# Performance work log

Measured on AMD Instinct MI355X. Metric: run time of the kernel, lower is better.

Reference implementation:

```python
import jax, jax.numpy as jnp
import numpy as np

N_STATE, N_CTRL, T, NB = 32, 16, 128, 64
NSC = N_STATE + N_CTRL

mT = lambda m: jnp.swapaxes(m, -1, -2)


def setup_inputs() -> dict:
    key = jax.random.key(0)
    k1, k2, k3, k4, k5, k6 = jax.random.split(key, 6)
    # Q must be PSD (the torch example builds Q = Qr^T Qr); add I for conditioning.
    Qr = jax.random.normal(k1, (NB, T, NSC, NSC), jnp.float32)
    Q = mT(Qr) @ Qr / NSC + jnp.eye(NSC, dtype=jnp.float32)
    p = jax.random.normal(k2, (NB, T, NSC), jnp.float32)
    x_init = jax.random.normal(k3, (NB, N_STATE), jnp.float32)
    # Stable-ish linear dynamics so the T=128 rollout does not blow up.
    A = jnp.tile(0.95 * jnp.eye(N_STATE, dtype=jnp.float32), (NB, 1, 1)) \
        + 0.02 * jax.random.normal(k4, (NB, N_STATE, N_STATE), jnp.float32)
    Bm = 0.1 * jax.random.normal(k5, (NB, N_STATE, N_CTRL), jnp.float32)
    c1 = 0.1 * jax.random.normal(k6, (NB, N_STATE), jnp.float32)
    return {"x_init": x_init, "Q": Q, "p": p, "A": A, "Bm": Bm, "c1": c1}


def _gains(Qt, qt, ns):
    # Qt: [B, nsc, nsc], qt: [B, nsc, 1]
    Qxx, Qxu = Qt[:, :ns, :ns], Qt[:, :ns, ns:]
    Qux, Quu = Qt[:, ns:, :ns], Qt[:, ns:, ns:]
    qx, qu = qt[:, :ns], qt[:, ns:]
    Quu_inv = jnp.linalg.pinv(Quu)          # batched pinv, as in the torch code
    K = -(Quu_inv @ Qux)                    # [B, nc, ns]
    k = -(Quu_inv @ qu)                     # [B, nc, 1]
    KT = mT(K)
    V = Qxx + Qxu @ K + KT @ Qux + KT @ Quu @ K
    v = qx + Qxu @ k + KT @ qu + KT @ Quu @ k
    return K, k, V, v


def _lqr(x_init, Q, p, A, Bm, c1):
    ns = A.shape[-1]
    F = jnp.concatenate([A, Bm], axis=-1)   # [B, ns, nsc]
    FT = mT(F)
    ft = c1[..., None]                       # [B, ns, 1]

    # ---- backward Riccati/DP recursion (sequential over T) ----
    K_last, k_last, V, v = _gains(Q[:, -1], p[:, -1][..., None], ns)

    def bstep(carry, inp):
        Vtp1, vtp1 = carry
        Qt_raw, pt = inp                     # [B,nsc,nsc], [B,nsc]
        Qt = Qt_raw + FT @ Vtp1 @ F
        qt = pt[..., None] + FT @ (Vtp1 @ ft) + FT @ vtp1
        K, k, Vt, vt = _gains(Qt, qt, ns)
        return (Vt, vt), (K, k)

    Qtm = jnp.swapaxes(Q[:, :-1], 0, 1)[::-1]   # [T-1, B, nsc, nsc], t = T-2..0
    ptm = jnp.swapaxes(p[:, :-1], 0, 1)[::-1]
    _, (Ks_rev, ks_rev) = jax.lax.scan(bstep, (V, v), (Qtm, ptm))
    Ks = jnp.concatenate([Ks_rev[::-1], K_last[None]], axis=0)  # [T, B, nc, ns], forward time order
    ks = jnp.concatenate([ks_rev[::-1], k_last[None]], axis=0)  # [T, B, nc, 1]

    # ---- forward rollout ----
    def fstep(x, inp):
        K, k, Qt, pt = inp
        u = jnp.einsum('bij,bj->bi', K, x) + k[..., 0]
        xu = jnp.concatenate([x, u], axis=-1)                 # tau_t, [B, nsc]
        obj = 0.5 * jnp.einsum('bi,bij,bj->b', xu, Qt, xu) + jnp.einsum('bi,bi->b', xu, pt)
        xn = jnp.einsum('bij,bj->bi', A, x) + jnp.einsum('bij,bj->bi', Bm, u) + c1
        return xn, (x, u, obj, xu)

    Qf = jnp.swapaxes(Q, 0, 1)               # [T, B, nsc, nsc]
    pf = jnp.swapaxes(p, 0, 1)
    _, (xs, us, objs, taus) = jax.lax.scan(fstep, x_init, (Ks, ks, Qf, pf))
    # xs: [T, B, ns] (x_0..x_{T-1}, matching torch which does not append x_T)
    return xs, us, objs, taus


def reference(x_init, Q, p, A, Bm, c1):
    return _lqr(x_init, Q, p, A, Bm, c1)
```

## Files before the change

kernel.cpp:

```cpp
#include <hip/hip_runtime.h>

#define TT     128
#define NBATCH 64

#define BAR()  asm volatile("s_waitcnt lgkmcnt(0)\n\ts_barrier" ::: "memory")
#define BARV() asm volatile("s_waitcnt vmcnt(0) lgkmcnt(0)\n\ts_barrier" ::: "memory")

__device__ __forceinline__ void gload16(const float* g, float* l) {
    __builtin_amdgcn_global_load_lds(
        (__attribute__((address_space(1))) void*)g,
        (__attribute__((address_space(3))) void*)l, 16, 0, 0);
}

__device__ __forceinline__ float rdlane(float v, int l) {
    return __int_as_float(__builtin_amdgcn_readlane(__float_as_int(v), l));
}

__device__ __forceinline__ void inv4(const float4 pr[4], float IP[4][4]) {
    float a00=pr[0].x, a01=pr[0].y, a10=pr[1].x, a11=pr[1].y;
    float b00=pr[0].z, b01=pr[0].w, b10=pr[1].z, b11=pr[1].w;
    float c00=pr[2].x, c01=pr[2].y, c10=pr[3].x, c11=pr[3].y;
    float d00=pr[2].z, d01=pr[2].w, d10=pr[3].z, d11=pr[3].w;
    float r = 1.0f / (a00*a11 - a01*a10);
    float ia00 =  a11*r, ia01 = -a01*r, ia10 = -a10*r, ia11 = a00*r;
    float t00 = ia00*b00 + ia01*b10, t01 = ia00*b01 + ia01*b11;
    float t10 = ia10*b00 + ia11*b10, t11 = ia10*b01 + ia11*b11;
    float u00 = c00*ia00 + c01*ia10, u01 = c00*ia01 + c01*ia11;
    float u10 = c10*ia00 + c11*ia10, u11 = c10*ia01 + c11*ia11;
    float s00 = d00 - (c00*t00 + c01*t10), s01 = d01 - (c00*t01 + c01*t11);
    float s10 = d10 - (c10*t00 + c11*t10), s11 = d11 - (c10*t01 + c11*t11);
    float rs = 1.0f / (s00*s11 - s01*s10);
    float is00 =  s11*rs, is01 = -s01*rs, is10 = -s10*rs, is11 = s00*rs;
    float su00 = is00*u00 + is01*u10, su01 = is00*u01 + is01*u11;
    float su10 = is10*u00 + is11*u10, su11 = is10*u01 + is11*u11;
    IP[0][0] = ia00 + (t00*su00 + t01*su10);
    IP[0][1] = ia01 + (t00*su01 + t01*su11);
    IP[1][0] = ia10 + (t10*su00 + t11*su10);
    IP[1][1] = ia11 + (t10*su01 + t11*su11);
    IP[0][2] = -(t00*is00 + t01*is10);  IP[0][3] = -(t00*is01 + t01*is11);
    IP[1][2] = -(t10*is00 + t11*is10);  IP[1][3] = -(t10*is01 + t11*is11);
    IP[2][0] = -su00; IP[2][1] = -su01;
    IP[3][0] = -su10; IP[3][1] = -su11;
    IP[2][2] = is00;  IP[2][3] = is01;
    IP[3][2] = is10;  IP[3][3] = is11;
}

__global__ __launch_bounds__(256, 1)
void lqr_backward(const float* __restrict__ Q, const float* __restrict__ p,
                  const float* __restrict__ A, const float* __restrict__ Bm,
                  const float* __restrict__ c1, float* __restrict__ Kws)
{
    const int b   = blockIdx.x;
    const int tid = threadIdx.x;

    __shared__ __align__(16) float Fs[32*52];
    __shared__ __align__(16) float Vs[32*36];
    __shared__ __align__(16) float Ms[32*52];
    __shared__ __align__(16) float Xs[48*52];
    __shared__ __align__(16) float Qtb[2][48*48];
    __shared__ __align__(16) float qtb[2][256];
    __shared__ __align__(16) float KKs[16*36];
    __shared__ float vsv[32], fts[32], wv[32];

    const int ar0 = (tid / 12) * 2, ac0 = (tid % 12) * 4;
    const int br0 = (tid / 12) * 4, bc0 = (tid % 12) * 4;
    const int pi  = (tid - 64) >> 2;
    const int pg  = (tid - 64) & 3;
    const int pj0 = pg * 8;

    for (int st = tid; st < 256; st += 256) {
        int k = st >> 3, q = st & 7;
        ((float4*)(Fs + k*52))[q] = ((const float4*)A)[(b*32 + k)*8 + q];
    }
    for (int st = tid; st < 128; st += 256) {
        int k = st >> 2, q = st & 3;
        ((float4*)(Fs + k*52))[8 + q] = ((const float4*)Bm)[(b*32 + k)*4 + q];
    }
    for (int st = tid; st < 288; st += 256) ((float4*)Vs)[st] = make_float4(0,0,0,0);
    if (tid < 32) { vsv[tid] = 0.0f; fts[tid] = c1[b*32 + tid]; }

    {
        const float* Qs0 = Q + (size_t)(b*TT + TT-1) * 2304;
        #pragma unroll
        for (int r = 0; r < 3; ++r) {
            int e = r*256 + tid;
            if (e < 576) gload16(Qs0 + e*4, Qtb[0] + e*4);
        }
        if (tid < 12) gload16(p + (size_t)(b*TT + TT-1)*48 + tid*4, qtb[0] + tid*4);
    }
    BARV();

    for (int t = TT-1; t >= 0; --t) {
        const int cur = (TT-1 - t) & 1;
        float* Qtc = Qtb[cur];
        float* qtc = qtb[cur];
        float* Kbase = Kws + (size_t)(b*TT + t) * 528;

        if (tid < 192) {
            float4 a0 = make_float4(0,0,0,0), a1 = a0;
            #pragma unroll
            for (int k = 0; k < 32; ++k) {
                float2 v = *(const float2*)(Vs + k*36 + ar0);
                float4 f = *(const float4*)(Fs + k*52 + ac0);
                a0.x += v.x*f.x; a0.y += v.x*f.y; a0.z += v.x*f.z; a0.w += v.x*f.w;
                a1.x += v.y*f.x; a1.y += v.y*f.y; a1.z += v.y*f.z; a1.w += v.y*f.w;
            }
            *(float4*)(Ms + (ar0  )*52 + ac0) = a0;
            *(float4*)(Ms + (ar0+1)*52 + ac0) = a1;
        } else {
            const int idx = tid - 192;
            if (t > 0) {
                const float* Qs = Q + (size_t)(b*TT + t-1) * 2304;
                float* dst = Qtb[cur ^ 1];
                #pragma unroll
                for (int r = 0; r < 9; ++r) {
                    int e = r*64 + idx;
                    gload16(Qs + e*4, dst + e*4);
                }
                if (idx < 12) gload16(p + (size_t)(b*TT + t-1)*48 + idx*4,
                                      qtb[cur ^ 1] + idx*4);
            }
            if (idx < 32) {
                float acc = vsv[idx];
                #pragma unroll
                for (int k = 0; k < 32; ++k) acc += Vs[idx*36 + k] * fts[k];
                wv[idx] = acc;
            }
        }
        BAR();

        if (tid < 144) {
            float4 a0 = *(const float4*)(Qtc + (br0+0)*48 + bc0);
            float4 a1 = *(const float4*)(Qtc + (br0+1)*48 + bc0);
            float4 a2 = *(const float4*)(Qtc + (br0+2)*48 + bc0);
            float4 a3 = *(const float4*)(Qtc + (br0+3)*48 + bc0);
            #pragma unroll
            for (int k = 0; k < 32; ++k) {
                float4 fr = *(const float4*)(Fs + k*52 + br0);
                float4 mc = *(const float4*)(Ms + k*52 + bc0);
                a0.x += fr.x*mc.x; a0.y += fr.x*mc.y; a0.z += fr.x*mc.z; a0.w += fr.x*mc.w;
                a1.x += fr.y*mc.x; a1.y += fr.y*mc.y; a1.z += fr.y*mc.z; a1.w += fr.y*mc.w;
                a2.x += fr.z*mc.x; a2.y += fr.z*mc.y; a2.z += fr.z*mc.z; a2.w += fr.z*mc.w;
                a3.x += fr.w*mc.x; a3.y += fr.w*mc.y; a3.z += fr.w*mc.z; a3.w += fr.w*mc.w;
            }
            *(float4*)(Xs + (br0+0)*52 + bc0) = a0;
            *(float4*)(Xs + (br0+1)*52 + bc0) = a1;
            *(float4*)(Xs + (br0+2)*52 + bc0) = a2;
            *(float4*)(Xs + (br0+3)*52 + bc0) = a3;
        } else if (tid >= 192 && tid < 240) {
            const int c = tid - 192;
            float acc = qtc[c];
            #pragma unroll
            for (int k = 0; k < 32; ++k) acc += Fs[k*52 + c] * wv[k];
            qtc[c] = acc;
            if (c >= 32) Xs[c*52 + 48] = acc;
        }
        BAR();

        float4 pa0, pa1; float pq[16];
        if (tid < 64) {
            const int c = (tid < 49) ? tid : 48;
            float col[16];
            #pragma unroll
            for (int r = 0; r < 16; ++r) col[r] = Xs[(32+r)*52 + c];

            #pragma unroll
            for (int q = 0; q < 4; ++q) {
                const int pc = 32 + 4*q;
                float4 pr[4];
                #pragma unroll
                for (int m = 0; m < 4; ++m) {
                    pr[m].x = rdlane(col[4*q+m], pc+0);
                    pr[m].y = rdlane(col[4*q+m], pc+1);
                    pr[m].z = rdlane(col[4*q+m], pc+2);
                    pr[m].w = rdlane(col[4*q+m], pc+3);
                }
                float IP[4][4];
                inv4(pr, IP);
                float R[4];
                #pragma unroll
                for (int m = 0; m < 4; ++m)
                    R[m] = IP[m][0]*col[4*q+0] + IP[m][1]*col[4*q+1]
                         + IP[m][2]*col[4*q+2] + IP[m][3]*col[4*q+3];
                #pragma unroll
                for (int r = 0; r < 16; ++r) {
                    if ((r >> 2) == q) continue;
                    float f0 = rdlane(col[r], pc+0);
                    float f1 = rdlane(col[r], pc+1);
                    float f2 = rdlane(col[r], pc+2);
                    float f3 = rdlane(col[r], pc+3);
                    col[r] -= f0*R[0] + f1*R[1] + f2*R[2] + f3*R[3];
                }
                #pragma unroll
                for (int m = 0; m < 4; ++m) col[4*q+m] = R[m];
            }

            if (tid < 32) {
                #pragma unroll
                for (int r = 0; r < 16; ++r) {
                    KKs[r*36 + c]    = col[r];
                    Kbase[c*16 + r]  = -col[r];
                }
            } else if (tid == 48) {
                #pragma unroll
                for (int r = 0; r < 16; ++r) {
                    KKs[r*36 + 32]   = col[r];
                    Kbase[512 + r]   = -col[r];
                }
            }
        } else if (tid < 192) {
            pa0 = *(const float4*)(Xs + pi*52 + pj0);
            pa1 = *(const float4*)(Xs + pi*52 + pj0 + 4);
            #pragma unroll
            for (int m = 0; m < 4; ++m) {
                float4 v4 = *(const float4*)(Xs + pi*52 + 32 + m*4);
                pq[m*4+0] = v4.x; pq[m*4+1] = v4.y;
                pq[m*4+2] = v4.z; pq[m*4+3] = v4.w;
            }
        }
        BAR();

        if (tid >= 64 && tid < 192) {
            #pragma unroll
            for (int k = 0; k < 16; ++k) {
                float4 k0 = *(const float4*)(KKs + k*36 + pj0);
                float4 k1 = *(const float4*)(KKs + k*36 + pj0 + 4);
                pa0.x -= pq[k]*k0.x; pa0.y -= pq[k]*k0.y;
                pa0.z -= pq[k]*k0.z; pa0.w -= pq[k]*k0.w;
                pa1.x -= pq[k]*k1.x; pa1.y -= pq[k]*k1.y;
                pa1.z -= pq[k]*k1.z; pa1.w -= pq[k]*k1.w;
            }
            *(float4*)(Vs + pi*36 + pj0)     = pa0;
            *(float4*)(Vs + pi*36 + pj0 + 4) = pa1;
            if (pg == 0) {
                float accv = qtc[pi];
                #pragma unroll
                for (int k = 0; k < 16; ++k) accv -= pq[k] * KKs[k*36 + 32];
                vsv[pi] = accv;
            }
        }
        BARV();
    }
}

__global__ __launch_bounds__(64, 1)
void lqr_forward(const float* __restrict__ Kws, const float* __restrict__ A,
                 const float* __restrict__ Bm, const float* __restrict__ c1,
                 const float* __restrict__ x_init,
                 float* __restrict__ xs, float* __restrict__ us,
                 float* __restrict__ taus)
{
    const int b = blockIdx.x, l = threadIdx.x;
    __shared__ __align__(16) float Fb[32*48];
    __shared__ __align__(16) float Kb[544];
    __shared__ float c1s[32], xu[48];

    for (int st = l; st < 256; st += 64) {
        int k = st >> 3, q = st & 7;
        ((float4*)Fb)[k*12 + q] = ((const float4*)A)[(b*32 + k)*8 + q];
    }
    for (int st = l; st < 128; st += 64) {
        int k = st >> 2, q = st & 3;
        ((float4*)Fb)[k*12 + 8 + q] = ((const float4*)Bm)[(b*32 + k)*4 + q];
    }
    if (l < 32) { c1s[l] = c1[b*32 + l]; xu[l] = x_init[b*32 + l]; }

    float4 ka, kb, kc = make_float4(0,0,0,0);
    {
        const float4* s0 = (const float4*)(Kws + (size_t)(b*TT) * 528);
        ka = s0[l]; kb = s0[l + 64];
        if (l < 4) kc = s0[l + 128];
    }
    __syncthreads();

    for (int t = 0; t < TT; ++t) {
        ((float4*)Kb)[l]      = ka;
        ((float4*)Kb)[l + 64] = kb;
        if (l < 4) ((float4*)Kb)[l + 128] = kc;
        __syncthreads();

        if (t + 1 < TT) {
            const float4* sn = (const float4*)(Kws + (size_t)(b*TT + t+1) * 528);
            ka = sn[l]; kb = sn[l + 64];
            if (l < 4) kc = sn[l + 128];
        }

        float part = 0.0f;
        int i = l & 15, g = l >> 4;
        #pragma unroll
        for (int jj = 0; jj < 8; ++jj) {
            int j = g*8 + jj;
            part += Kb[j*16 + i] * xu[j];
        }
        part += __shfl_down(part, 32);
        part += __shfl_down(part, 16);
        float ui = part + Kb[512 + i];
        if (l < 16) {
            xu[32 + l] = ui;
            us[(size_t)(t*64 + b)*16 + l] = ui;
        }
        __syncthreads();

        if (l < 32) xs[(size_t)(t*64 + b)*32 + l] = xu[l];
        if (l < 48) taus[(size_t)(t*64 + b)*48 + l] = xu[l];

        float pn = 0.0f;
        int i2 = l & 31, h = l >> 5;
        #pragma unroll
        for (int jj = 0; jj < 24; ++jj) {
            int j = h*24 + jj;
            pn += Fb[i2*48 + j] * xu[j];
        }
        pn += __shfl_down(pn, 32);
        float xni = pn + ((l < 32) ? c1s[i2] : 0.0f);
        __syncthreads();
        if (l < 32) xu[l] = xni;
        __syncthreads();
    }
}

__global__ __launch_bounds__(256, 4)
void lqr_obj(const float* __restrict__ Q, const float* __restrict__ p,
             const float* __restrict__ taus, float* __restrict__ objs)
{
    const int bi = blockIdx.x;
    const int b = bi >> 7, t = bi & 127;
    const int tid = threadIdx.x;
    __shared__ float xu[48];
    __shared__ float red[8];
    const float* tp = taus + (size_t)(t*64 + b)*48;
    if (tid < 48) xu[tid] = tp[tid];
    __syncthreads();

    const float4* Q4 = (const float4*)(Q + (size_t)bi * 2304);
    float acc = 0.0f;
    for (int e4 = tid; e4 < 576; e4 += 256) {
        float4 qv = Q4[e4];
        int r = e4 / 12, c = (e4 % 12) * 4;
        float xr = xu[r];
        acc += xr * (qv.x*xu[c] + qv.y*xu[c+1] + qv.z*xu[c+2] + qv.w*xu[c+3]);
    }
    acc *= 0.5f;
    if (tid < 48) acc += xu[tid] * p[(size_t)bi*48 + tid];

    #pragma unroll
    for (int off = 32; off > 0; off >>= 1) acc += __shfl_down(acc, off);
    if ((tid & 63) == 0) red[tid >> 6] = acc;
    __syncthreads();
    if (tid == 0) objs[(t << 6) + b] = red[0] + red[1] + red[2] + red[3];
}

extern "C" void kernel_launch(void* const* d_in, const int* in_sizes, int n_in,
                              void* d_out, int out_size, void* d_ws, size_t ws_size,
                              hipStream_t stream) {
    const float* x_init = (const float*)d_in[0];
    const float* Q      = (const float*)d_in[1];
    const float* p      = (const float*)d_in[2];
    const float* A      = (const float*)d_in[3];
    const float* Bm     = (const float*)d_in[4];
    const float* c1     = (const float*)d_in[5];

    float* out  = (float*)d_out;
    float* xs   = out;
    float* us   = out + 262144;
    float* objs = out + 393216;
    float* taus = out + 401408;

    float* Kws = (float*)d_ws;

    lqr_backward<<<NBATCH, 256, 0, stream>>>(Q, p, A, Bm, c1, Kws);
    lqr_forward<<<NBATCH, 64, 0, stream>>>(Kws, A, Bm, c1, x_init, xs, us, taus);
    lqr_obj<<<NBATCH*TT, 256, 0, stream>>>(Q, p, taus, objs);
}
```

Measured before the change: 696.7 us.

## Rebalance per-thread work in Riccati backward pass across all 256 threads

The V·F product is now computed by 96 threads with 4x4 register tiles instead of 192 threads with 2x4 tiles. The V update (Xs minus Q_xu·K) is spread over all 256 threads with 4 outputs each instead of 128 threads with 8. Threads 0-63 load their operands after the gain barrier because they are busy with the inverse before it. The aim is to shorten the critical path of each sequential timestep by using idle threads, at the cost of extra LDS reads after the barrier for the first wave.

```diff
diff --git a/kernel.cpp b/kernel.cpp
--- a/kernel.cpp
+++ b/kernel.cpp
@@ -62,11 +62,11 @@
     __shared__ __align__(16) float KKs[16*36];
     __shared__ float vsv[32], fts[32], wv[32];
 
-    const int ar0 = (tid / 12) * 2, ac0 = (tid % 12) * 4;
+    const int ai0 = (tid / 12) * 4, ac0 = (tid % 12) * 4;
     const int br0 = (tid / 12) * 4, bc0 = (tid % 12) * 4;
-    const int pi  = (tid - 64) >> 2;
-    const int pg  = (tid - 64) & 3;
-    const int pj0 = pg * 8;
+    const int pi  = tid >> 3;
+    const int pg  = tid & 7;
+    const int pj0 = pg * 4;
 
     for (int st = tid; st < 256; st += 256) {
         int k = st >> 3, q = st & 7;
@@ -96,18 +96,22 @@
         float* qtc = qtb[cur];
         float* Kbase = Kws + (size_t)(b*TT + t) * 528;
 
-        if (tid < 192) {
-            float4 a0 = make_float4(0,0,0,0), a1 = a0;
+        if (tid < 96) {
+            float4 a0 = make_float4(0,0,0,0), a1 = a0, a2 = a0, a3 = a0;
             #pragma unroll
             for (int k = 0; k < 32; ++k) {
-                float2 v = *(const float2*)(Vs + k*36 + ar0);
+                float4 v = *(const float4*)(Vs + k*36 + ai0);
                 float4 f = *(const float4*)(Fs + k*52 + ac0);
                 a0.x += v.x*f.x; a0.y += v.x*f.y; a0.z += v.x*f.z; a0.w += v.x*f.w;
                 a1.x += v.y*f.x; a1.y += v.y*f.y; a1.z += v.y*f.z; a1.w += v.y*f.w;
-            }
-            *(float4*)(Ms + (ar0  )*52 + ac0) = a0;
-            *(float4*)(Ms + (ar0+1)*52 + ac0) = a1;
-        } else {
+                a2.x += v.z*f.x; a2.y += v.z*f.y; a2.z += v.z*f.z; a2.w += v.z*f.w;
+                a3.x += v.w*f.x; a3.y += v.w*f.y; a3.z += v.w*f.z; a3.w += v.w*f.w;
+            }
+            *(float4*)(Ms + (ai0+0)*52 + ac0) = a0;
+            *(float4*)(Ms + (ai0+1)*52 + ac0) = a1;
+            *(float4*)(Ms + (ai0+2)*52 + ac0) = a2;
+            *(float4*)(Ms + (ai0+3)*52 + ac0) = a3;
+        } else if (tid >= 192) {
             const int idx = tid - 192;
             if (t > 0) {
                 const float* Qs = Q + (size_t)(b*TT + t-1) * 2304;
@@ -157,7 +161,7 @@
         }
         BAR();
 
-        float4 pa0, pa1; float pq[16];
+        float4 pa0; float pq[16];
         if (tid < 64) {
             const int c = (tid < 49) ? tid : 48;
             float col[16];
@@ -208,9 +212,8 @@
                     Kbase[512 + r]   = -col[r];
                 }
             }
-        } else if (tid < 192) {
+        } else {
             pa0 = *(const float4*)(Xs + pi*52 + pj0);
-            pa1 = *(const float4*)(Xs + pi*52 + pj0 + 4);
             #pragma unroll
             for (int m = 0; m < 4; ++m) {
                 float4 v4 = *(const float4*)(Xs + pi*52 + 32 + m*4);
@@ -220,18 +223,23 @@
         }
         BAR();
 
-        if (tid >= 64 && tid < 192) {
+        {
+            if (tid < 64) {
+                pa0 = *(const float4*)(Xs + pi*52 + pj0);
+                #pragma unroll
+                for (int m = 0; m < 4; ++m) {
+                    float4 v4 = *(const float4*)(Xs + pi*52 + 32 + m*4);
+                    pq[m*4+0] = v4.x; pq[m*4+1] = v4.y;
+                    pq[m*4+2] = v4.z; pq[m*4+3] = v4.w;
+                }
+            }
             #pragma unroll
             for (int k = 0; k < 16; ++k) {
                 float4 k0 = *(const float4*)(KKs + k*36 + pj0);
-                float4 k1 = *(const float4*)(KKs + k*36 + pj0 + 4);
                 pa0.x -= pq[k]*k0.x; pa0.y -= pq[k]*k0.y;
                 pa0.z -= pq[k]*k0.z; pa0.w -= pq[k]*k0.w;
-                pa1.x -= pq[k]*k1.x; pa1.y -= pq[k]*k1.y;
-                pa1.z -= pq[k]*k1.z; pa1.w -= pq[k]*k1.w;
-            }
-            *(float4*)(Vs + pi*36 + pj0)     = pa0;
-            *(float4*)(Vs + pi*36 + pj0 + 4) = pa1;
+            }
+            *(float4*)(Vs + pi*36 + pj0) = pa0;
             if (pg == 0) {
                 float accv = qtc[pi];
                 #pragma unroll
```

Result: no change. 684.9 us, median of 3 (-1.7%).
